# Performance work log

Measured on AMD Instinct MI355X. Metric: run time of the kernel, lower is better.

Reference implementation:

```python
import jax, jax.numpy as jnp
import numpy as np

NU, NM, FEAT, E, EL, H, ED, C = 50000, 20000, 32, 262144, 100000, 512, 7, 7


def _seg_mean(msg, dst, n):
    # scatter-mean aggregation (PyG SAGEConv default aggr='mean'; empty segments -> 0)
    s = jax.ops.segment_sum(msg, dst, num_segments=n)
    cnt = jax.ops.segment_sum(jnp.ones(dst.shape, msg.dtype), dst, num_segments=n)
    return s / jnp.maximum(cnt, 1.0)[:, None]


def _conv(x_src, x_dst, ei, ea, lw, lb, rw, ew, eb):
    # EdgeSAGEConv: message = x_j + edge_lin(edge_attr); out = lin_l(mean-aggr) + lin_r(x_dst)
    msg = x_src[ei[0]] + ea @ ew + eb            # [E, H]
    agg = _seg_mean(msg, ei[1], x_dst.shape[0])  # [N_dst, H]
    return agg @ lw + lb + x_dst @ rw


def setup_inputs() -> dict:
    key = jax.random.key(0)
    ks = iter(jax.random.split(key, 40))

    def rn(shape, scale=1.0):
        return jax.random.normal(next(ks), shape, jnp.float32) * scale

    inp = {}
    inp["movie_x"] = rn((NM, FEAT))
    inp["user_emb_w"] = rn((NU, H))
    inp["movie_emb_w"] = rn((NM, H))
    inp["movie_lin_w"] = rn((FEAT, H), FEAT ** -0.5)
    inp["movie_lin_b"] = jnp.zeros((H,), jnp.float32)
    inp["edge_attr_um"] = rn((E, ED))
    inp["edge_attr_mu"] = rn((E, ED))
    for p in ("mu1", "um1", "mu2", "um2"):
        inp[p + "_lin_l_w"] = rn((H, H), H ** -0.5)
        inp[p + "_lin_l_b"] = jnp.zeros((H,), jnp.float32)
        inp[p + "_lin_r_w"] = rn((H, H), H ** -0.5)
        inp[p + "_edge_w"] = rn((ED, H), ED ** -0.5)
        inp[p + "_edge_b"] = jnp.zeros((H,), jnp.float32)
    inp["cls_w"] = rn((2 * H, C), (2 * H) ** -0.5)
    inp["cls_b"] = jnp.zeros((C,), jnp.float32)
    inp["edge_index_um"] = jnp.stack([
        jax.random.randint(next(ks), (E,), 0, NU),
        jax.random.randint(next(ks), (E,), 0, NM)])
    inp["edge_index_mu"] = jnp.stack([
        jax.random.randint(next(ks), (E,), 0, NM),
        jax.random.randint(next(ks), (E,), 0, NU)])
    inp["edge_label_index"] = jnp.stack([
        jax.random.randint(next(ks), (EL,), 0, NU),
        jax.random.randint(next(ks), (EL,), 0, NM)])
    return inp


def reference(movie_x, user_emb_w, movie_emb_w, movie_lin_w, movie_lin_b,
              edge_attr_um, edge_attr_mu,
              mu1_lin_l_w, mu1_lin_l_b, mu1_lin_r_w, mu1_edge_w, mu1_edge_b,
              um1_lin_l_w, um1_lin_l_b, um1_lin_r_w, um1_edge_w, um1_edge_b,
              mu2_lin_l_w, mu2_lin_l_b, mu2_lin_r_w, mu2_edge_w, mu2_edge_b,
              um2_lin_l_w, um2_lin_l_b, um2_lin_r_w, um2_edge_w, um2_edge_b,
              cls_w, cls_b,
              edge_index_um, edge_index_mu, edge_label_index):
    # node encoders (node_id == arange -> embedding table used directly)
    x_u = user_emb_w                                             # [NU, H]
    x_m = movie_x @ movie_lin_w + movie_lin_b + movie_emb_w      # [NM, H]
    # hetero layer 1 (one edge type per destination node type)
    u1 = jax.nn.relu(_conv(x_m, x_u, edge_index_mu, edge_attr_mu,
                           mu1_lin_l_w, mu1_lin_l_b, mu1_lin_r_w, mu1_edge_w, mu1_edge_b))
    m1 = jax.nn.relu(_conv(x_u, x_m, edge_index_um, edge_attr_um,
                           um1_lin_l_w, um1_lin_l_b, um1_lin_r_w, um1_edge_w, um1_edge_b))
    # hetero layer 2
    u2 = _conv(m1, u1, edge_index_mu, edge_attr_mu,
               mu2_lin_l_w, mu2_lin_l_b, mu2_lin_r_w, mu2_edge_w, mu2_edge_b)
    m2 = _conv(u1, m1, edge_index_um, edge_attr_um,
               um2_lin_l_w, um2_lin_l_b, um2_lin_r_w, um2_edge_w, um2_edge_b)
    # edge classifier
    feat = jnp.concatenate([u2[edge_label_index[0]], m2[edge_label_index[1]]], axis=-1)
    return feat @ cls_w + cls_b
```

## Files before the change

kernel.cpp:

```cpp
#include <hip/hip_runtime.h>
#include <hip/hip_bf16.h>

#define NUU 50000
#define NMM 20000
#define NT (NUU + NMM)
#define FEAT 32
#define NE 262144
#define NEL 100000
#define HD 512
#define EDIM 7
#define NC 7

typedef __hip_bfloat16 bf16;
typedef __attribute__((ext_vector_type(8))) short short8;
typedef __attribute__((ext_vector_type(4))) float f32x4;

__device__ __forceinline__ float b2f(unsigned short u)
{
  return __uint_as_float((unsigned)u << 16);
}
__device__ __forceinline__ unsigned short f2bbits(float x)
{
  __hip_bfloat16 h = __float2bfloat16(x);
  return *reinterpret_cast<unsigned short*>(&h);
}
__device__ __forceinline__ float2 ld2(const float* p) { return *(const float2*)p; }
__device__ __forceinline__ void st2b(bf16* p, float x, float y)
{
  ushort2 u = make_ushort2(f2bbits(x), f2bbits(y));
  *(ushort2*)p = u;
}
__device__ __forceinline__ void gload16(const void* g, void* l)
{
  __builtin_amdgcn_global_load_lds(
      (const __attribute__((address_space(1))) void*)g,
      (__attribute__((address_space(3))) void*)l, 16, 0, 0);
}

__global__ __launch_bounds__(256) void phase1_k(
    const float* __restrict__ mx, const float* __restrict__ W,
    const float* __restrict__ b, const float* __restrict__ emb,
    bf16* __restrict__ xm, const float* __restrict__ uin, bf16* __restrict__ ubf,
    const float* __restrict__ lwA, const float* __restrict__ rwA, bf16* __restrict__ WcA,
    const float* __restrict__ lwB, const float* __restrict__ rwB, bf16* __restrict__ WcB,
    const int* __restrict__ dmu, const int* __restrict__ dum, int* __restrict__ cnt)
{
  const int tid = threadIdx.x;
  const int bx = blockIdx.x;
  if (bx < 1024) {
    const int c0 = 2 * tid;
    float2 wreg[FEAT];
#pragma unroll
    for (int k = 0; k < FEAT; ++k) wreg[k] = ld2(&W[(size_t)k * HD + c0]);
    const float2 bv = ld2(&b[c0]);
    __shared__ float xr[FEAT];
    for (int m = bx; m < NMM; m += 1024) {
      if (tid < FEAT) xr[tid] = mx[(size_t)m * FEAT + tid];
      __syncthreads();
      float2 e2 = ld2(&emb[(size_t)m * HD + c0]);
      float s0 = bv.x + e2.x, s1 = bv.y + e2.y;
#pragma unroll
      for (int k = 0; k < FEAT; ++k) {
        s0 += xr[k] * wreg[k].x;
        s1 += xr[k] * wreg[k].y;
      }
      st2b(&xm[(size_t)m * HD + c0], s0, s1);
      __syncthreads();
    }
  } else if (bx < 2048) {
    const int n4 = NUU * HD / 4;
    for (int i = (bx - 1024) * 256 + tid; i < n4; i += 1024 * 256) {
      float4 v = *(const float4*)&uin[4 * (size_t)i];
      ushort4 u = make_ushort4(f2bbits(v.x), f2bbits(v.y), f2bbits(v.z), f2bbits(v.w));
      *(ushort4*)&ubf[4 * (size_t)i] = u;
    }
  } else if (bx < 3072) {
    const int b2 = bx - 2048;
    const int side = b2 >> 9;
    const int rem = b2 & 511;
    const float* lw = side ? lwB : lwA;
    const float* rw = side ? rwB : rwA;
    bf16* Wcat = side ? WcB : WcA;
    __shared__ float s[32][33];
    const int tx = tid & 31;
    const int ty = tid >> 5;
    const int nt = (rem & 15) * 32;
    const int kt = (rem >> 4) * 32;
#pragma unroll
    for (int q = 0; q < 4; ++q) {
      int k = kt + q * 8 + ty;
      int n = nt + tx;
      float v = (k < HD) ? lw[(size_t)k * HD + n] : rw[(size_t)(k - HD) * HD + n];
      s[q * 8 + ty][tx] = v;
    }
    __syncthreads();
#pragma unroll
    for (int q = 0; q < 4; ++q) {
      int n = nt + q * 8 + ty;
      int k = kt + tx;
      Wcat[(size_t)n * (2 * HD) + k] = __float2bfloat16(s[tx][q * 8 + ty]);
    }
  } else {
    for (int i = (bx - 3072) * 256 + tid; i < NE; i += 1024 * 256) {
      atomicAdd(&cnt[dmu[i]], 1);
      atomicAdd(&cnt[NUU + dum[i]], 1);
    }
  }
}

__global__ __launch_bounds__(512) void scanA_projw_k(
    const int* __restrict__ in, int* __restrict__ out, int* __restrict__ bsum, int n,
    int GN,
    const float* __restrict__ lwA, const float* __restrict__ rwA,
    const float* __restrict__ lbA,
    const float* __restrict__ lwB, const float* __restrict__ rwB,
    const float* __restrict__ lbB, const float* __restrict__ clsW,
    float* __restrict__ WlA, float* __restrict__ WrA, float* __restrict__ ccA,
    float* __restrict__ WlB, float* __restrict__ WrB, float* __restrict__ ccB)
{
  const int tid = threadIdx.x;
  if ((int)blockIdx.x < GN) {
    __shared__ int s[512];
    const int i = blockIdx.x * 512 + tid;
    int v = (i < n) ? in[i] : 0;
    s[tid] = v;
    __syncthreads();
    for (int d = 1; d < 512; d <<= 1) {
      int t = (tid >= d) ? s[tid - d] : 0;
      __syncthreads();
      s[tid] += t;
      __syncthreads();
    }
    if (i < n) out[i] = s[tid] - v;
    if (tid == 511) bsum[blockIdx.x] = s[511];
    return;
  }
  const int unit = (blockIdx.x - GN) * 8 + (tid >> 6);
  if (unit >= 2 * (HD + 1)) return;
  const int side = unit / (HD + 1);
  const int k = unit % (HD + 1);
  const int l = tid & 63;
  const float* lw = side ? lwB : lwA;
  const float* rw = side ? rwB : rwA;
  const float* lb = side ? lbB : lbA;
  const float* cw = clsW + (side ? (size_t)HD * NC : 0);
  float* Wl = side ? WlB : WlA;
  float* Wr = side ? WrB : WrA;
  float* cc = side ? ccB : ccA;
  if (k < HD) {
    float aL[NC] = {0, 0, 0, 0, 0, 0, 0};
    float aR[NC] = {0, 0, 0, 0, 0, 0, 0};
    for (int j = l; j < HD; j += 64) {
      float a = lw[(size_t)k * HD + j];
      float b = rw[(size_t)k * HD + j];
#pragma unroll
      for (int c = 0; c < NC; ++c) {
        float w = cw[(size_t)j * NC + c];
        aL[c] += a * w;
        aR[c] += b * w;
      }
    }
#pragma unroll
    for (int c = 0; c < NC; ++c)
      for (int s2 = 32; s2; s2 >>= 1) {
        aL[c] += __shfl_xor(aL[c], s2);
        aR[c] += __shfl_xor(aR[c], s2);
      }
    if (l == 0) {
#pragma unroll
      for (int c = 0; c < NC; ++c) {
        Wl[k * NC + c] = aL[c];
        Wr[k * NC + c] = aR[c];
      }
    }
  } else {
    float a0[NC] = {0, 0, 0, 0, 0, 0, 0};
    for (int j = l; j < HD; j += 64) {
      float a = lb[j];
#pragma unroll
      for (int c = 0; c < NC; ++c) a0[c] += a * cw[(size_t)j * NC + c];
    }
#pragma unroll
    for (int c = 0; c < NC; ++c)
      for (int s2 = 32; s2; s2 >>= 1) a0[c] += __shfl_xor(a0[c], s2);
    if (l == 0) {
#pragma unroll
      for (int c = 0; c < NC; ++c) cc[c] = a0[c];
    }
  }
}

__global__ __launch_bounds__(256) void scanB_p2w2t_k(
    int* __restrict__ bsum, int nb,
    const float* __restrict__ ewA, const float* __restrict__ ebA,
    const float* __restrict__ WlA, float* __restrict__ ewPA, float* __restrict__ ebPA,
    const float* __restrict__ ewB, const float* __restrict__ ebB,
    const float* __restrict__ WlB, float* __restrict__ ewPB, float* __restrict__ ebPB,
    const float* __restrict__ WAu, const float* __restrict__ WBu, bf16* __restrict__ W2u,
    const float* __restrict__ WAm, const float* __restrict__ WBm, bf16* __restrict__ W2m)
{
  const int tid = threadIdx.x;
  if (blockIdx.x == 0) {
    __shared__ int s[256];
    int v = (tid < nb) ? bsum[tid] : 0;
    s[tid] = v;
    __syncthreads();
    for (int d = 1; d < 256; d <<= 1) {
      int t = (tid >= d) ? s[tid - d] : 0;
      __syncthreads();
      s[tid] += t;
      __syncthreads();
    }
    if (tid < nb) bsum[tid] = s[tid] - v;
    return;
  }
  const int b = blockIdx.x - 1;
  if (b < 4) {
    const int side = b >> 1;
    const float* ew = side ? ewB : ewA;
    const float* ebv = side ? ebB : ebA;
    const float* Wl = side ? WlB : WlA;
    float* ewP = side ? ewPB : ewPA;
    float* ebP = side ? ebPB : ebPA;
    const int j = (b & 1) * 4 + (tid >> 6);
    const int l = tid & 63;
    const float* __restrict__ src = (j < 7) ? &ew[(size_t)j * HD] : ebv;
    float acc[NC] = {0, 0, 0, 0, 0, 0, 0};
    for (int k = l; k < HD; k += 64) {
      float v = src[k];
#pragma unroll
      for (int c = 0; c < NC; ++c) acc[c] += v * Wl[(size_t)k * NC + c];
    }
#pragma unroll
    for (int c = 0; c < NC; ++c)
      for (int s2 = 32; s2; s2 >>= 1) acc[c] += __shfl_xor(acc[c], s2);
    if (l == 0) {
      if (j < 7) {
#pragma unroll
        for (int c = 0; c < NC; ++c) ewP[j * 8 + c] = acc[c];
        ewP[j * 8 + 7] = 0.f;
      } else {
#pragma unroll
        for (int c = 0; c < NC; ++c) ebP[c] = acc[c];
        ebP[7] = 0.f;
      }
    }
  } else {
    int idx = (b - 4) * 256 + tid;
    const int side = idx >= 16 * HD;
    if (side) idx -= 16 * HD;
    const float* WA = side ? WAm : WAu;
    const float* WB = side ? WBm : WBu;
    bf16* W2t = side ? W2m : W2u;
    int n = idx >> 9;
    int k = idx & (HD - 1);
    float v = 0.f;
    if (n < 7) v = WA[k * NC + n];
    else if (n >= 8 && n < 15) v = WB[k * NC + (n - 8)];
    W2t[(size_t)n * HD + k] = __float2bfloat16(v);
  }
}

__global__ __launch_bounds__(512) void scan_c512(int* __restrict__ out,
                                                 const int* __restrict__ bsum, int n)
{
  const int i = blockIdx.x * 512 + threadIdx.x;
  if (i < n) out[i] += bsum[blockIdx.x];
}

__global__ void fill2_k(const int* __restrict__ smu, const int* __restrict__ dmu,
                        const int* __restrict__ sum_, const int* __restrict__ dum,
                        const int* __restrict__ off, int* __restrict__ fill,
                        int2* __restrict__ csr2)
{
  for (int i = blockIdx.x * blockDim.x + threadIdx.x; i < NE; i += gridDim.x * blockDim.x) {
    int d0 = dmu[i];
    int p0 = off[d0] + atomicAdd(&fill[d0], 1);
    csr2[p0] = make_int2(smu[i], i);
    int d1 = NUU + dum[i];
    int p1 = off[d1] + atomicAdd(&fill[d1], 1);
    csr2[p1] = make_int2(sum_[i], i);
  }
}

__global__ __launch_bounds__(256) void spmm_all_k(
    const bf16* __restrict__ x_m, const bf16* __restrict__ ue_bf,
    const int2* __restrict__ csr2, const int* __restrict__ off,
    const int* __restrict__ cnt,
    const float* __restrict__ eaMU, const float* __restrict__ eaUM,
    const float* __restrict__ ew_u, const float* __restrict__ eb_u,
    const float* __restrict__ ew_m, const float* __restrict__ eb_m,
    float* __restrict__ eaSum, bf16* __restrict__ t)
{
  const int lane = threadIdx.x & 63;
  const int d = blockIdx.x * 4 + (threadIdx.x >> 6);
  if (d >= NT) return;
  const int user = (d < NUU);
  const bf16* __restrict__ xsrc = user ? x_m : ue_bf;
  const float* __restrict__ eaG = user ? eaMU : eaUM;
  const float* __restrict__ ew = user ? ew_u : ew_m;
  const float* __restrict__ eb = user ? eb_u : eb_m;
  const int deg = cnt[d];
  const int start = off[d];
  const int c0 = lane * 8;
  float acc[8] = {0.f, 0.f, 0.f, 0.f, 0.f, 0.f, 0.f, 0.f};
  float eacc = 0.f;
  int i = 0;
  for (; i + 3 < deg; i += 4) {
    int2 e0 = csr2[start + i], e1 = csr2[start + i + 1];
    int2 e2 = csr2[start + i + 2], e3 = csr2[start + i + 3];
    short8 v0 = *(const short8*)&xsrc[(size_t)e0.x * HD + c0];
    short8 v1 = *(const short8*)&xsrc[(size_t)e1.x * HD + c0];
    short8 v2 = *(const short8*)&xsrc[(size_t)e2.x * HD + c0];
    short8 v3 = *(const short8*)&xsrc[(size_t)e3.x * HD + c0];
    if (lane < 7)
      eacc += (eaG[(size_t)e0.y * EDIM + lane] + eaG[(size_t)e1.y * EDIM + lane]) +
              (eaG[(size_t)e2.y * EDIM + lane] + eaG[(size_t)e3.y * EDIM + lane]);
#pragma unroll
    for (int j = 0; j < 8; ++j)
      acc[j] += (b2f((unsigned short)v0[j]) + b2f((unsigned short)v1[j])) +
                (b2f((unsigned short)v2[j]) + b2f((unsigned short)v3[j]));
  }
  for (; i < deg; ++i) {
    int2 e = csr2[start + i];
    short8 v = *(const short8*)&xsrc[(size_t)e.x * HD + c0];
    if (lane < 7) eacc += eaG[(size_t)e.y * EDIM + lane];
#pragma unroll
    for (int j = 0; j < 8; ++j) acc[j] += b2f((unsigned short)v[j]);
  }
  if (lane < 8) eaSum[(size_t)d * 8 + lane] = (lane < 7) ? eacc : 0.f;
  short8 sv;
  if (deg > 0) {
    const float inv = 1.f / (float)deg;
    float es[8] = {0.f, 0.f, 0.f, 0.f, 0.f, 0.f, 0.f, 0.f};
#pragma unroll
    for (int j = 0; j < NC; ++j) {
      const float av = __shfl(eacc, j);
      const float* __restrict__ wr = &ew[(size_t)j * HD + c0];
#pragma unroll
      for (int jj = 0; jj < 8; ++jj) es[jj] += av * wr[jj];
    }
#pragma unroll
    for (int jj = 0; jj < 8; ++jj)
      sv[jj] = (short)f2bbits((acc[jj] + es[jj]) * inv + eb[c0 + jj]);
  } else {
#pragma unroll
    for (int jj = 0; jj < 8; ++jj) sv[jj] = (short)f2bbits(0.f);
  }
  *(short8*)&t[(size_t)d * HD + c0] = sv;
}

__global__ __launch_bounds__(256) void agg_all_k(
    const float* __restrict__ Pab, const int2* __restrict__ csr2,
    const int* __restrict__ off, const int* __restrict__ cnt,
    const float* __restrict__ eaSum,
    const float* __restrict__ ewP_u, const float* __restrict__ ebP_u,
    const float* __restrict__ cc_u, const float* __restrict__ ewP_m,
    const float* __restrict__ ebP_m, const float* __restrict__ cc_m,
    float* __restrict__ Pu, float* __restrict__ Pm)
{
  const int g = threadIdx.x >> 3;
  const int cl = threadIdx.x & 7;
  const int d = blockIdx.x * 32 + g;
  if (d >= NT) return;
  const int user = (d < NUU);
  const size_t srcbase = user ? (size_t)NUU : 0;
  const float* ewP = user ? ewP_u : ewP_m;
  const float* ebP = user ? ebP_u : ebP_m;
  const float* cc = user ? cc_u : cc_m;
  float* P = user ? Pu : Pm;
  const int dl = user ? d : d - NUU;
  const int deg = cnt[d];
  const int start = off[d];
  float a = 0.f;
  int i = 0;
  for (; i + 1 < deg; i += 2) {
    int s0 = csr2[start + i].x, s1 = csr2[start + i + 1].x;
    a += Pab[(srcbase + s0) * 16 + cl] + Pab[(srcbase + s1) * 16 + cl];
  }
  if (i < deg) a += Pab[(srcbase + csr2[start + i].x) * 16 + cl];
  float r = Pab[(size_t)d * 16 + 8 + cl] + ((cl < 7) ? cc[cl] : 0.f);
  if (deg > 0) {
    float inv = 1.f / (float)deg;
    float es = 0.f;
#pragma unroll
    for (int j = 0; j < NC; ++j) es += eaSum[(size_t)d * 8 + j] * ewP[j * 8 + cl];
    r += (a + es) * inv + ebP[cl];
  }
  if (cl < 7) P[(size_t)dl * NC + cl] = r;
}

__global__ __launch_bounds__(256) void gemm_all_k(
    const bf16* __restrict__ tbuf, const bf16* __restrict__ ue_bf,
    const bf16* __restrict__ x_m, const bf16* __restrict__ Wcat_u,
    const bf16* __restrict__ Wcat_m, const float* __restrict__ bias_u,
    const float* __restrict__ bias_m, const bf16* __restrict__ W2t_u,
    const bf16* __restrict__ W2t_m, float* __restrict__ Pab, int nwgU)
{
  __shared__ __align__(16) char lds[34816];
  const int tid = threadIdx.x;
  const int lane = tid & 63;
  const int wid = tid >> 6;
  const int wr = wid >> 1, wc = wid & 1;
  const int lr = lane & 15, lk = lane >> 4;

  const int nwg = gridDim.x;
  const int orig = blockIdx.x;
  const int q = nwg >> 3, r8 = nwg & 7;
  const int xcd = orig & 7, pos = orig >> 3;
  const int wg = (xcd < r8) ? xcd * (q + 1) + pos : r8 * (q + 1) + (xcd - r8) * q + pos;

  const int user = (wg < nwgU);
  const int wl = user ? wg : wg - nwgU;
  const bf16* __restrict__ A1 = user ? tbuf : tbuf + (size_t)NUU * HD;
  const bf16* __restrict__ A2 = user ? ue_bf : x_m;
  const bf16* __restrict__ Wcat = user ? Wcat_u : Wcat_m;
  const float* __restrict__ bias = user ? bias_u : bias_m;
  const bf16* __restrict__ W2t = user ? W2t_u : W2t_m;
  const int M = user ? NUU : NMM;
  const size_t rowbase = user ? 0 : (size_t)NUU;

  const int mt = wl >> 2, nt = wl & 3;
  const int m0 = mt * 128;
  const int n0 = nt * 128;

  const int srow = tid >> 2;
  const int sslot = tid & 3;

  f32x4 acc[4][4];
#pragma unroll
  for (int i = 0; i < 4; ++i)
#pragma unroll
    for (int j = 0; j < 4; ++j) acc[i][j] = (f32x4){0.f, 0.f, 0.f, 0.f};

  int gr0 = m0 + srow;       if (gr0 >= M) gr0 = M - 1;
  int gr1 = m0 + srow + 64;  if (gr1 >= M) gr1 = M - 1;
  const size_t aoff0 = (size_t)gr0 * HD + 8 * sslot;
  const size_t aoff1 = (size_t)gr1 * HD + 8 * sslot;
  const size_t boff0 = (size_t)(n0 + srow) * (2 * HD) + 8 * sslot;
  const size_t boff1 = (size_t)(n0 + srow + 64) * (2 * HD) + 8 * sslot;

  for (int ks = 0; ks < 32; ++ks) {
    const int k0 = ks * 32;
    const bf16* __restrict__ Ap = (k0 < HD) ? A1 : A2;
    const int ac = k0 & (HD - 1);
    gload16(Ap + aoff0 + ac, &lds[tid * 16]);
    gload16(Ap + aoff1 + ac, &lds[4096 + tid * 16]);
    gload16(Wcat + boff0 + k0, &lds[8192 + tid * 16]);
    gload16(Wcat + boff1 + k0, &lds[12288 + tid * 16]);
    __syncthreads();

    short8 af[4], bfr[4];
#pragma unroll
    for (int mf = 0; mf < 4; ++mf)
      af[mf] = *(const short8*)&lds[(wr * 64 + mf * 16 + lr) * 64 + lk * 16];
#pragma unroll
    for (int nf = 0; nf < 4; ++nf)
      bfr[nf] = *(const short8*)&lds[8192 + (wc * 64 + nf * 16 + lr) * 64 + lk * 16];
#pragma unroll
    for (int mf = 0; mf < 4; ++mf)
#pragma unroll
      for (int nf = 0; nf < 4; ++nf)
        acc[mf][nf] = __builtin_amdgcn_mfma_f32_16x16x32_bf16(
            af[mf], bfr[nf], acc[mf][nf], 0, 0, 0);
    __syncthreads();
  }

  bf16* zs = (bf16*)lds;
  const int ZLD = 136;
#pragma unroll
  for (int nf = 0; nf < 4; ++nf) {
    const int col_l = wc * 64 + nf * 16 + lr;
    const float bv = bias[n0 + col_l];
#pragma unroll
    for (int mf = 0; mf < 4; ++mf) {
      const int row_l = wr * 64 + mf * 16 + lk * 4;
#pragma unroll
      for (int r = 0; r < 4; ++r) {
        float v = fmaxf(acc[mf][nf][r] + bv, 0.f);
        zs[(size_t)(row_l + r) * ZLD + col_l] = __float2bfloat16(v);
      }
    }
  }
  __syncthreads();

  const int strip = wid * 32;
  f32x4 p0 = {0.f, 0.f, 0.f, 0.f}, p1 = {0.f, 0.f, 0.f, 0.f};
#pragma unroll
  for (int kk = 0; kk < 4; ++kk) {
    short8 bfg = *(const short8*)&W2t[(size_t)lr * HD + n0 + kk * 32 + 8 * lk];
    short8 a0 = *(const short8*)&zs[(size_t)(strip + lr) * ZLD + kk * 32 + 8 * lk];
    short8 a1 = *(const short8*)&zs[(size_t)(strip + 16 + lr) * ZLD + kk * 32 + 8 * lk];
    p0 = __builtin_amdgcn_mfma_f32_16x16x32_bf16(a0, bfg, p0, 0, 0, 0);
    p1 = __builtin_amdgcn_mfma_f32_16x16x32_bf16(a1, bfg, p1, 0, 0, 0);
  }
#pragma unroll
  for (int r = 0; r < 4; ++r) {
    int row0 = m0 + strip + lk * 4 + r;
    if (row0 < M) atomicAdd(&Pab[(rowbase + row0) * 16 + lr], p0[r]);
    int row1 = m0 + strip + 16 + lk * 4 + r;
    if (row1 < M) atomicAdd(&Pab[(rowbase + row1) * 16 + lr], p1[r]);
  }
}

__global__ void gather_out_k(const float* __restrict__ Pu, const float* __restrict__ Pm,
                             const int* __restrict__ eli, const float* __restrict__ cb,
                             float* __restrict__ out)
{
  const int i = blockIdx.x * 256 + threadIdx.x;
  if (i >= NEL * NC) return;
  int e = i / NC;
  int c = i - e * NC;
  out[i] = Pu[(size_t)eli[e] * NC + c] + Pm[(size_t)eli[NEL + e] * NC + c] + cb[c];
}

static inline char* bump(char*& p, size_t bytes)
{
  char* r = p;
  p += (bytes + 255) & ~(size_t)255;
  return r;
}

extern "C" void kernel_launch(void* const* d_in, const int* in_sizes, int n_in,
                              void* d_out, int out_size, void* d_ws, size_t ws_size,
                              hipStream_t stream)
{
  const float* movie_x   = (const float*)d_in[0];
  const float* user_emb  = (const float*)d_in[1];
  const float* movie_emb = (const float*)d_in[2];
  const float* mlw       = (const float*)d_in[3];
  const float* mlb       = (const float*)d_in[4];
  const float* ea_um     = (const float*)d_in[5];
  const float* ea_mu     = (const float*)d_in[6];
  const float* mu1_lw = (const float*)d_in[7];
  const float* mu1_lb = (const float*)d_in[8];
  const float* mu1_rw = (const float*)d_in[9];
  const float* mu1_ew = (const float*)d_in[10];
  const float* mu1_eb = (const float*)d_in[11];
  const float* um1_lw = (const float*)d_in[12];
  const float* um1_lb = (const float*)d_in[13];
  const float* um1_rw = (const float*)d_in[14];
  const float* um1_ew = (const float*)d_in[15];
  const float* um1_eb = (const float*)d_in[16];
  const float* mu2_lw = (const float*)d_in[17];
  const float* mu2_lb = (const float*)d_in[18];
  const float* mu2_rw = (const float*)d_in[19];
  const float* mu2_ew = (const float*)d_in[20];
  const float* mu2_eb = (const float*)d_in[21];
  const float* um2_lw = (const float*)d_in[22];
  const float* um2_lb = (const float*)d_in[23];
  const float* um2_rw = (const float*)d_in[24];
  const float* um2_ew = (const float*)d_in[25];
  const float* um2_eb = (const float*)d_in[26];
  const float* cls_w  = (const float*)d_in[27];
  const float* cls_b  = (const float*)d_in[28];
  const int*   ei_um  = (const int*)d_in[29];
  const int*   ei_mu  = (const int*)d_in[30];
  const int*   eli    = (const int*)d_in[31];
  float* out = (float*)d_out;

  char* w = (char*)d_ws;
  char* zbase = w;
  int* cf     = (int*)bump(w, (size_t)2 * NT * 4);
  int* cnt    = cf;
  int* fill   = cf + NT;
  float* Pab  = (float*)bump(w, (size_t)NT * 16 * 4);
  size_t zbytes = (size_t)(w - zbase);
  float* eaSum = (float*)bump(w, (size_t)NT * 8 * 4);
  bf16* x_m   = (bf16*)bump(w, (size_t)NMM * HD * 2);
  bf16* tbuf  = (bf16*)bump(w, (size_t)NT * HD * 2);
  bf16* ue_bf = (bf16*)bump(w, (size_t)NUU * HD * 2);
  bf16* Wcat_u1 = (bf16*)bump(w, (size_t)HD * 2 * HD * 2);
  bf16* Wcat_m1 = (bf16*)bump(w, (size_t)HD * 2 * HD * 2);
  float* Pu   = (float*)bump(w, (size_t)NUU * NC * 4);
  float* Pm   = (float*)bump(w, (size_t)NMM * NC * 4);
  float* Wl_u = (float*)bump(w, (size_t)HD * NC * 4);
  float* Wr_u = (float*)bump(w, (size_t)HD * NC * 4);
  float* cc_u = (float*)bump(w, 64 * 4);
  float* Wl_m = (float*)bump(w, (size_t)HD * NC * 4);
  float* Wr_m = (float*)bump(w, (size_t)HD * NC * 4);
  float* cc_m = (float*)bump(w, 64 * 4);
  bf16* W2t_u = (bf16*)bump(w, (size_t)16 * HD * 2);
  bf16* W2t_m = (bf16*)bump(w, (size_t)16 * HD * 2);
  float* ewP_u = (float*)bump(w, 64 * 4);
  float* ebP_u = (float*)bump(w, 64 * 4);
  float* ewP_m = (float*)bump(w, 64 * 4);
  float* ebP_m = (float*)bump(w, 64 * 4);
  int* off    = (int*)bump(w, (size_t)NT * 4);
  int* bsum   = (int*)bump(w, 256 * 4);
  int2* csr2  = (int2*)bump(w, (size_t)2 * NE * 8);

  const int GN = (NT + 511) / 512;
  const int PJB = (2 * (HD + 1) + 7) / 8;

  hipMemsetAsync(zbase, 0, zbytes, stream);

  phase1_k<<<4096, 256, 0, stream>>>(movie_x, mlw, mlb, movie_emb, x_m,
                                     user_emb, ue_bf,
                                     mu1_lw, mu1_rw, Wcat_u1,
                                     um1_lw, um1_rw, Wcat_m1,
                                     ei_mu + NE, ei_um + NE, cnt);

  scanA_projw_k<<<GN + PJB, 512, 0, stream>>>(cnt, off, bsum, NT, GN,
                                              mu2_lw, mu2_rw, mu2_lb,
                                              um2_lw, um2_rw, um2_lb, cls_w,
                                              Wl_u, Wr_u, cc_u, Wl_m, Wr_m, cc_m);

  scanB_p2w2t_k<<<69, 256, 0, stream>>>(bsum, GN,
                                        mu2_ew, mu2_eb, Wl_u, ewP_u, ebP_u,
                                        um2_ew, um2_eb, Wl_m, ewP_m, ebP_m,
                                        Wl_m, Wr_u, W2t_u, Wl_u, Wr_m, W2t_m);

  scan_c512<<<GN, 512, 0, stream>>>(off, bsum, NT);
  fill2_k<<<1024, 256, 0, stream>>>(ei_mu, ei_mu + NE, ei_um, ei_um + NE,
                                    off, fill, csr2);

  spmm_all_k<<<(NT + 3) / 4, 256, 0, stream>>>(x_m, ue_bf, csr2, off, cnt,
                                               ea_mu, ea_um,
                                               mu1_ew, mu1_eb, um1_ew, um1_eb,
                                               eaSum, tbuf);

  const int nwgU = ((NUU + 127) / 128) * 4;
  const int nwgM = ((NMM + 127) / 128) * 4;
  gemm_all_k<<<nwgU + nwgM, 256, 0, stream>>>(tbuf, ue_bf, x_m, Wcat_u1, Wcat_m1,
                                              mu1_lb, um1_lb, W2t_u, W2t_m,
                                              Pab, nwgU);

  agg_all_k<<<(NT + 31) / 32, 256, 0, stream>>>(Pab, csr2, off, cnt, eaSum,
                                                ewP_u, ebP_u, cc_u,
                                                ewP_m, ebP_m, cc_m, Pu, Pm);

  gather_out_k<<<(NEL * NC + 255) / 256, 256, 0, stream>>>(Pu, Pm, eli, cls_b, out);
}
```

Baseline: 330.6 us.

## Overlap CSR fill, SpMM and GEMM across user/movie halves via fused kernels

Splits the CSR fill, the SpMM and the GEMM into user and movie halves. Independent work from different stages now runs in the same launch: the movie-side CSR fill runs alongside the user SpMM, and the movie SpMM runs alongside the user GEMM. The GEMM epilogue is also reworked to stage the ReLU output in LDS in two passes, which halves LDS usage (17 KB instead of 34 KB) and should allow higher occupancy. The cost is an extra launch, more branch-divergent heterogeneous blocks, and a serial final GEMM over only the movie rows.

```diff
diff --git a/kernel.cpp b/kernel.cpp
--- a/kernel.cpp
+++ b/kernel.cpp
@@ -268,33 +268,36 @@
   if (i < n) out[i] += bsum[blockIdx.x];
 }
 
-__global__ void fill2_k(const int* __restrict__ smu, const int* __restrict__ dmu,
-                        const int* __restrict__ sum_, const int* __restrict__ dum,
+__device__ __forceinline__ void fill_half(const int* __restrict__ src,
+                                          const int* __restrict__ dst, int dofs,
+                                          const int* __restrict__ off,
+                                          int* __restrict__ fill,
+                                          int2* __restrict__ csr2,
+                                          int bx, int nblocks, int tid)
+{
+  for (int i = bx * 256 + tid; i < NE; i += nblocks * 256) {
+    int d = dofs + dst[i];
+    int p = off[d] + atomicAdd(&fill[d], 1);
+    csr2[p] = make_int2(src[i], i);
+  }
+}
+
+__global__ void fillu_k(const int* __restrict__ smu, const int* __restrict__ dmu,
                         const int* __restrict__ off, int* __restrict__ fill,
                         int2* __restrict__ csr2)
 {
-  for (int i = blockIdx.x * blockDim.x + threadIdx.x; i < NE; i += gridDim.x * blockDim.x) {
-    int d0 = dmu[i];
-    int p0 = off[d0] + atomicAdd(&fill[d0], 1);
-    csr2[p0] = make_int2(smu[i], i);
-    int d1 = NUU + dum[i];
-    int p1 = off[d1] + atomicAdd(&fill[d1], 1);
-    csr2[p1] = make_int2(sum_[i], i);
-  }
-}
-
-__global__ __launch_bounds__(256) void spmm_all_k(
-    const bf16* __restrict__ x_m, const bf16* __restrict__ ue_bf,
+  fill_half(smu, dmu, 0, off, fill, csr2, blockIdx.x, gridDim.x, threadIdx.x);
+}
+
+__device__ __forceinline__ void spmm_body(
+    int d, const bf16* __restrict__ x_m, const bf16* __restrict__ ue_bf,
     const int2* __restrict__ csr2, const int* __restrict__ off,
     const int* __restrict__ cnt,
     const float* __restrict__ eaMU, const float* __restrict__ eaUM,
     const float* __restrict__ ew_u, const float* __restrict__ eb_u,
     const float* __restrict__ ew_m, const float* __restrict__ eb_m,
-    float* __restrict__ eaSum, bf16* __restrict__ t)
-{
-  const int lane = threadIdx.x & 63;
-  const int d = blockIdx.x * 4 + (threadIdx.x >> 6);
-  if (d >= NT) return;
+    float* __restrict__ eaSum, bf16* __restrict__ t, int lane)
+{
   const int user = (d < NUU);
   const bf16* __restrict__ xsrc = user ? x_m : ue_bf;
   const float* __restrict__ eaG = user ? eaMU : eaUM;
@@ -350,6 +353,152 @@
   *(short8*)&t[(size_t)d * HD + c0] = sv;
 }
 
+__global__ __launch_bounds__(256) void spmmU_fillM_k(
+    const bf16* __restrict__ x_m, const bf16* __restrict__ ue_bf,
+    const int2* __restrict__ csr2, const int* __restrict__ off,
+    const int* __restrict__ cnt,
+    const float* __restrict__ eaMU, const float* __restrict__ eaUM,
+    const float* __restrict__ ew_u, const float* __restrict__ eb_u,
+    const float* __restrict__ ew_m, const float* __restrict__ eb_m,
+    float* __restrict__ eaSum, bf16* __restrict__ t, int nspmm,
+    const int* __restrict__ sum_, const int* __restrict__ dum,
+    int* __restrict__ fill, int2* __restrict__ csr2w)
+{
+  if ((int)blockIdx.x < nspmm) {
+    const int d = blockIdx.x * 4 + (threadIdx.x >> 6);
+    if (d < NUU)
+      spmm_body(d, x_m, ue_bf, csr2, off, cnt, eaMU, eaUM,
+                ew_u, eb_u, ew_m, eb_m, eaSum, t, threadIdx.x & 63);
+  } else {
+    fill_half(sum_, dum, NUU, off, fill, csr2w,
+              blockIdx.x - nspmm, gridDim.x - nspmm, threadIdx.x);
+  }
+}
+
+__device__ __forceinline__ void gemm_body(
+    const bf16* __restrict__ A1, const bf16* __restrict__ A2,
+    const bf16* __restrict__ Wcat, const float* __restrict__ bias,
+    const bf16* __restrict__ W2t, float* __restrict__ Pab,
+    int M, size_t rowbase, int orig, int nwg, char* lds)
+{
+  const int tid = threadIdx.x;
+  const int lane = tid & 63;
+  const int wid = tid >> 6;
+  const int wr = wid >> 1, wc = wid & 1;
+  const int lr = lane & 15, lk = lane >> 4;
+
+  const int q = nwg >> 3, r8 = nwg & 7;
+  const int xcd = orig & 7, pos = orig >> 3;
+  const int wg = (xcd < r8) ? xcd * (q + 1) + pos : r8 * (q + 1) + (xcd - r8) * q + pos;
+
+  const int mt = wg >> 2, nt = wg & 3;
+  const int m0 = mt * 128;
+  const int n0 = nt * 128;
+
+  const int srow = tid >> 2;
+  const int sslot = tid & 3;
+
+  f32x4 acc[4][4];
+#pragma unroll
+  for (int i = 0; i < 4; ++i)
+#pragma unroll
+    for (int j = 0; j < 4; ++j) acc[i][j] = (f32x4){0.f, 0.f, 0.f, 0.f};
+
+  int gr0 = m0 + srow;       if (gr0 >= M) gr0 = M - 1;
+  int gr1 = m0 + srow + 64;  if (gr1 >= M) gr1 = M - 1;
+  const size_t aoff0 = (size_t)gr0 * HD + 8 * sslot;
+  const size_t aoff1 = (size_t)gr1 * HD + 8 * sslot;
+  const size_t boff0 = (size_t)(n0 + srow) * (2 * HD) + 8 * sslot;
+  const size_t boff1 = (size_t)(n0 + srow + 64) * (2 * HD) + 8 * sslot;
+
+  for (int ks = 0; ks < 32; ++ks) {
+    const int k0 = ks * 32;
+    const bf16* __restrict__ Ap = (k0 < HD) ? A1 : A2;
+    const int ac = k0 & (HD - 1);
+    gload16(Ap + aoff0 + ac, &lds[tid * 16]);
+    gload16(Ap + aoff1 + ac, &lds[4096 + tid * 16]);
+    gload16(Wcat + boff0 + k0, &lds[8192 + tid * 16]);
+    gload16(Wcat + boff1 + k0, &lds[12288 + tid * 16]);
+    __syncthreads();
+
+    short8 af[4], bfr[4];
+#pragma unroll
+    for (int mf = 0; mf < 4; ++mf)
+      af[mf] = *(const short8*)&lds[(wr * 64 + mf * 16 + lr) * 64 + lk * 16];
+#pragma unroll
+    for (int nf = 0; nf < 4; ++nf)
+      bfr[nf] = *(const short8*)&lds[8192 + (wc * 64 + nf * 16 + lr) * 64 + lk * 16];
+#pragma unroll
+    for (int mf = 0; mf < 4; ++mf)
+#pragma unroll
+      for (int nf = 0; nf < 4; ++nf)
+        acc[mf][nf] = __builtin_amdgcn_mfma_f32_16x16x32_bf16(
+            af[mf], bfr[nf], acc[mf][nf], 0, 0, 0);
+    __syncthreads();
+  }
+
+  bf16* zs = (bf16*)lds;
+  const int ZLD = 136;
+#pragma unroll
+  for (int pass = 0; pass < 2; ++pass) {
+    if (wr == pass) {
+#pragma unroll
+      for (int nf = 0; nf < 4; ++nf) {
+        const int col_l = wc * 64 + nf * 16 + lr;
+        const float bv = bias[n0 + col_l];
+#pragma unroll
+        for (int mf = 0; mf < 4; ++mf) {
+          const int row_l = mf * 16 + lk * 4;
+#pragma unroll
+          for (int r = 0; r < 4; ++r) {
+            float v = fmaxf(acc[mf][nf][r] + bv, 0.f);
+            zs[(size_t)(row_l + r) * ZLD + col_l] = __float2bfloat16(v);
+          }
+        }
+      }
+    }
+    __syncthreads();
+    f32x4 p0 = {0.f, 0.f, 0.f, 0.f};
+#pragma unroll
+    for (int kk = 0; kk < 4; ++kk) {
+      short8 bfg = *(const short8*)&W2t[(size_t)lr * HD + n0 + kk * 32 + 8 * lk];
+      short8 a0 = *(const short8*)&zs[(size_t)(wid * 16 + lr) * ZLD + kk * 32 + 8 * lk];
+      p0 = __builtin_amdgcn_mfma_f32_16x16x32_bf16(a0, bfg, p0, 0, 0, 0);
+    }
+#pragma unroll
+    for (int r = 0; r < 4; ++r) {
+      int row = m0 + pass * 64 + wid * 16 + lk * 4 + r;
+      if (row < M) atomicAdd(&Pab[(rowbase + row) * 16 + lr], p0[r]);
+    }
+    __syncthreads();
+  }
+}
+
+__global__ __launch_bounds__(256) void gemm_spmm_k(
+    const bf16* __restrict__ A1, const bf16* __restrict__ A2,
+    const bf16* __restrict__ Wcat, const float* __restrict__ bias,
+    const bf16* __restrict__ W2t, float* __restrict__ Pab, int M, int rowbase,
+    int nwgGemm,
+    const bf16* __restrict__ x_m, const bf16* __restrict__ ue_bf,
+    const int2* __restrict__ csr2, const int* __restrict__ off,
+    const int* __restrict__ cnt,
+    const float* __restrict__ eaMU, const float* __restrict__ eaUM,
+    const float* __restrict__ ew_u, const float* __restrict__ eb_u,
+    const float* __restrict__ ew_m, const float* __restrict__ eb_m,
+    float* __restrict__ eaSum, bf16* __restrict__ t, int dbase)
+{
+  __shared__ __align__(16) char lds[17408];
+  if ((int)blockIdx.x < nwgGemm) {
+    gemm_body(A1, A2, Wcat, bias, W2t, Pab, M, (size_t)rowbase,
+              blockIdx.x, nwgGemm, lds);
+  } else {
+    const int d = dbase + (blockIdx.x - nwgGemm) * 4 + (threadIdx.x >> 6);
+    if (d < NT)
+      spmm_body(d, x_m, ue_bf, csr2, off, cnt, eaMU, eaUM,
+                ew_u, eb_u, ew_m, eb_m, eaSum, t, threadIdx.x & 63);
+  }
+}
+
 __global__ __launch_bounds__(256) void agg_all_k(
     const float* __restrict__ Pab, const int2* __restrict__ csr2,
     const int* __restrict__ off, const int* __restrict__ cnt,
@@ -388,119 +537,6 @@
     r += (a + es) * inv + ebP[cl];
   }
   if (cl < 7) P[(size_t)dl * NC + cl] = r;
-}
-
-__global__ __launch_bounds__(256) void gemm_all_k(
-    const bf16* __restrict__ tbuf, const bf16* __restrict__ ue_bf,
-    const bf16* __restrict__ x_m, const bf16* __restrict__ Wcat_u,
-    const bf16* __restrict__ Wcat_m, const float* __restrict__ bias_u,
-    const float* __restrict__ bias_m, const bf16* __restrict__ W2t_u,
-    const bf16* __restrict__ W2t_m, float* __restrict__ Pab, int nwgU)
-{
-  __shared__ __align__(16) char lds[34816];
-  const int tid = threadIdx.x;
-  const int lane = tid & 63;
-  const int wid = tid >> 6;
-  const int wr = wid >> 1, wc = wid & 1;
-  const int lr = lane & 15, lk = lane >> 4;
-
-  const int nwg = gridDim.x;
-  const int orig = blockIdx.x;
-  const int q = nwg >> 3, r8 = nwg & 7;
-  const int xcd = orig & 7, pos = orig >> 3;
-  const int wg = (xcd < r8) ? xcd * (q + 1) + pos : r8 * (q + 1) + (xcd - r8) * q + pos;
-
-  const int user = (wg < nwgU);
-  const int wl = user ? wg : wg - nwgU;
-  const bf16* __restrict__ A1 = user ? tbuf : tbuf + (size_t)NUU * HD;
-  const bf16* __restrict__ A2 = user ? ue_bf : x_m;
-  const bf16* __restrict__ Wcat = user ? Wcat_u : Wcat_m;
-  const float* __restrict__ bias = user ? bias_u : bias_m;
-  const bf16* __restrict__ W2t = user ? W2t_u : W2t_m;
-  const int M = user ? NUU : NMM;
-  const size_t rowbase = user ? 0 : (size_t)NUU;
-
-  const int mt = wl >> 2, nt = wl & 3;
-  const int m0 = mt * 128;
-  const int n0 = nt * 128;
-
-  const int srow = tid >> 2;
-  const int sslot = tid & 3;
-
-  f32x4 acc[4][4];
-#pragma unroll
-  for (int i = 0; i < 4; ++i)
-#pragma unroll
-    for (int j = 0; j < 4; ++j) acc[i][j] = (f32x4){0.f, 0.f, 0.f, 0.f};
-
-  int gr0 = m0 + srow;       if (gr0 >= M) gr0 = M - 1;
-  int gr1 = m0 + srow + 64;  if (gr1 >= M) gr1 = M - 1;
-  const size_t aoff0 = (size_t)gr0 * HD + 8 * sslot;
-  const size_t aoff1 = (size_t)gr1 * HD + 8 * sslot;
-  const size_t boff0 = (size_t)(n0 + srow) * (2 * HD) + 8 * sslot;
-  const size_t boff1 = (size_t)(n0 + srow + 64) * (2 * HD) + 8 * sslot;
-
-  for (int ks = 0; ks < 32; ++ks) {
-    const int k0 = ks * 32;
-    const bf16* __restrict__ Ap = (k0 < HD) ? A1 : A2;
-    const int ac = k0 & (HD - 1);
-    gload16(Ap + aoff0 + ac, &lds[tid * 16]);
-    gload16(Ap + aoff1 + ac, &lds[4096 + tid * 16]);
-    gload16(Wcat + boff0 + k0, &lds[8192 + tid * 16]);
-    gload16(Wcat + boff1 + k0, &lds[12288 + tid * 16]);
-    __syncthreads();
-
-    short8 af[4], bfr[4];
-#pragma unroll
-    for (int mf = 0; mf < 4; ++mf)
-      af[mf] = *(const short8*)&lds[(wr * 64 + mf * 16 + lr) * 64 + lk * 16];
-#pragma unroll
-    for (int nf = 0; nf < 4; ++nf)
-      bfr[nf] = *(const short8*)&lds[8192 + (wc * 64 + nf * 16 + lr) * 64 + lk * 16];
-#pragma unroll
-    for (int mf = 0; mf < 4; ++mf)
-#pragma unroll
-      for (int nf = 0; nf < 4; ++nf)
-        acc[mf][nf] = __builtin_amdgcn_mfma_f32_16x16x32_bf16(
-            af[mf], bfr[nf], acc[mf][nf], 0, 0, 0);
-    __syncthreads();
-  }
-
-  bf16* zs = (bf16*)lds;
-  const int ZLD = 136;
-#pragma unroll
-  for (int nf = 0; nf < 4; ++nf) {
-    const int col_l = wc * 64 + nf * 16 + lr;
-    const float bv = bias[n0 + col_l];
-#pragma unroll
-    for (int mf = 0; mf < 4; ++mf) {
-      const int row_l = wr * 64 + mf * 16 + lk * 4;
-#pragma unroll
-      for (int r = 0; r < 4; ++r) {
-        float v = fmaxf(acc[mf][nf][r] + bv, 0.f);
-        zs[(size_t)(row_l + r) * ZLD + col_l] = __float2bfloat16(v);
-      }
-    }
-  }
-  __syncthreads();
-
-  const int strip = wid * 32;
-  f32x4 p0 = {0.f, 0.f, 0.f, 0.f}, p1 = {0.f, 0.f, 0.f, 0.f};
-#pragma unroll
-  for (int kk = 0; kk < 4; ++kk) {
-    short8 bfg = *(const short8*)&W2t[(size_t)lr * HD + n0 + kk * 32 + 8 * lk];
-    short8 a0 = *(const short8*)&zs[(size_t)(strip + lr) * ZLD + kk * 32 + 8 * lk];
-    short8 a1 = *(const short8*)&zs[(size_t)(strip + 16 + lr) * ZLD + kk * 32 + 8 * lk];
-    p0 = __builtin_amdgcn_mfma_f32_16x16x32_bf16(a0, bfg, p0, 0, 0, 0);
-    p1 = __builtin_amdgcn_mfma_f32_16x16x32_bf16(a1, bfg, p1, 0, 0, 0);
-  }
-#pragma unroll
-  for (int r = 0; r < 4; ++r) {
-    int row0 = m0 + strip + lk * 4 + r;
-    if (row0 < M) atomicAdd(&Pab[(rowbase + row0) * 16 + lr], p0[r]);
-    int row1 = m0 + strip + 16 + lk * 4 + r;
-    if (row1 < M) atomicAdd(&Pab[(rowbase + row1) * 16 + lr], p1[r]);
-  }
 }
 
 __global__ void gather_out_k(const float* __restrict__ Pu, const float* __restrict__ Pm,
@@ -612,19 +648,27 @@
                                         Wl_m, Wr_u, W2t_u, Wl_u, Wr_m, W2t_m);
 
   scan_c512<<<GN, 512, 0, stream>>>(off, bsum, NT);
-  fill2_k<<<1024, 256, 0, stream>>>(ei_mu, ei_mu + NE, ei_um, ei_um + NE,
-                                    off, fill, csr2);
-
-  spmm_all_k<<<(NT + 3) / 4, 256, 0, stream>>>(x_m, ue_bf, csr2, off, cnt,
-                                               ea_mu, ea_um,
-                                               mu1_ew, mu1_eb, um1_ew, um1_eb,
-                                               eaSum, tbuf);
+
+  fillu_k<<<1024, 256, 0, stream>>>(ei_mu, ei_mu + NE, off, fill, csr2);
+
+  const int nspmmU = (NUU + 3) / 4;
+  spmmU_fillM_k<<<nspmmU + 512, 256, 0, stream>>>(
+      x_m, ue_bf, csr2, off, cnt, ea_mu, ea_um,
+      mu1_ew, mu1_eb, um1_ew, um1_eb, eaSum, tbuf, nspmmU,
+      ei_um, ei_um + NE, fill, csr2);
 
   const int nwgU = ((NUU + 127) / 128) * 4;
+  const int nspmmM = (NMM + 3) / 4;
+  gemm_spmm_k<<<nwgU + nspmmM, 256, 0, stream>>>(
+      tbuf, ue_bf, Wcat_u1, mu1_lb, W2t_u, Pab, NUU, 0, nwgU,
+      x_m, ue_bf, csr2, off, cnt, ea_mu, ea_um,
+      mu1_ew, mu1_eb, um1_ew, um1_eb, eaSum, tbuf, NUU);
+
   const int nwgM = ((NMM + 127) / 128) * 4;
-  gemm_all_k<<<nwgU + nwgM, 256, 0, stream>>>(tbuf, ue_bf, x_m, Wcat_u1, Wcat_m1,
-                                              mu1_lb, um1_lb, W2t_u, W2t_m,
-                                              Pab, nwgU);
+  gemm_spmm_k<<<nwgM, 256, 0, stream>>>(
+      tbuf + (size_t)NUU * HD, x_m, Wcat_m1, um1_lb, W2t_m, Pab, NMM, NUU, nwgM,
+      x_m, ue_bf, csr2, off, cnt, ea_mu, ea_um,
+      mu1_ew, mu1_eb, um1_ew, um1_eb, eaSum, tbuf, NT);
 
   agg_all_k<<<(NT + 31) / 32, 256, 0, stream>>>(Pab, csr2, off, cnt, eaSum,
                                                 ewP_u, ebP_u, cc_u,
```

Result: slower. 348.0 us (+5.2%).

## Split CSR fill by edge type and overlap movie fill with user SpMM

Applied to the files above, without the earlier changes.

The combined CSR fill kernel is split into a user-destination fill and a movie-destination fill. The movie fill now runs as extra blocks inside the user-side SpMM kernel, and a separate kernel handles the movie-side SpMM afterwards. The goal is to hide the atomic scatter of the second fill behind the gather-heavy user aggregation. The cost is one more kernel launch and blocks with uneven work sharing the GPU. The gemm kernel is only moved within the file.

```diff
diff --git a/kernel.cpp b/kernel.cpp
--- a/kernel.cpp
+++ b/kernel.cpp
@@ -268,33 +268,36 @@
   if (i < n) out[i] += bsum[blockIdx.x];
 }
 
-__global__ void fill2_k(const int* __restrict__ smu, const int* __restrict__ dmu,
-                        const int* __restrict__ sum_, const int* __restrict__ dum,
+__device__ __forceinline__ void fill_half(const int* __restrict__ src,
+                                          const int* __restrict__ dst, int dofs,
+                                          const int* __restrict__ off,
+                                          int* __restrict__ fill,
+                                          int2* __restrict__ csr2,
+                                          int bx, int nblocks, int tid)
+{
+  for (int i = bx * 256 + tid; i < NE; i += nblocks * 256) {
+    int d = dofs + dst[i];
+    int p = off[d] + atomicAdd(&fill[d], 1);
+    csr2[p] = make_int2(src[i], i);
+  }
+}
+
+__global__ void fillu_k(const int* __restrict__ smu, const int* __restrict__ dmu,
                         const int* __restrict__ off, int* __restrict__ fill,
                         int2* __restrict__ csr2)
 {
-  for (int i = blockIdx.x * blockDim.x + threadIdx.x; i < NE; i += gridDim.x * blockDim.x) {
-    int d0 = dmu[i];
-    int p0 = off[d0] + atomicAdd(&fill[d0], 1);
-    csr2[p0] = make_int2(smu[i], i);
-    int d1 = NUU + dum[i];
-    int p1 = off[d1] + atomicAdd(&fill[d1], 1);
-    csr2[p1] = make_int2(sum_[i], i);
-  }
-}
-
-__global__ __launch_bounds__(256) void spmm_all_k(
-    const bf16* __restrict__ x_m, const bf16* __restrict__ ue_bf,
+  fill_half(smu, dmu, 0, off, fill, csr2, blockIdx.x, gridDim.x, threadIdx.x);
+}
+
+__device__ __forceinline__ void spmm_body(
+    int d, const bf16* __restrict__ x_m, const bf16* __restrict__ ue_bf,
     const int2* __restrict__ csr2, const int* __restrict__ off,
     const int* __restrict__ cnt,
     const float* __restrict__ eaMU, const float* __restrict__ eaUM,
     const float* __restrict__ ew_u, const float* __restrict__ eb_u,
     const float* __restrict__ ew_m, const float* __restrict__ eb_m,
-    float* __restrict__ eaSum, bf16* __restrict__ t)
-{
-  const int lane = threadIdx.x & 63;
-  const int d = blockIdx.x * 4 + (threadIdx.x >> 6);
-  if (d >= NT) return;
+    float* __restrict__ eaSum, bf16* __restrict__ t, int lane)
+{
   const int user = (d < NUU);
   const bf16* __restrict__ xsrc = user ? x_m : ue_bf;
   const float* __restrict__ eaG = user ? eaMU : eaUM;
@@ -350,6 +353,156 @@
   *(short8*)&t[(size_t)d * HD + c0] = sv;
 }
 
+__global__ __launch_bounds__(256) void spmmU_fillM_k(
+    const bf16* __restrict__ x_m, const bf16* __restrict__ ue_bf,
+    const int2* __restrict__ csr2, const int* __restrict__ off,
+    const int* __restrict__ cnt,
+    const float* __restrict__ eaMU, const float* __restrict__ eaUM,
+    const float* __restrict__ ew_u, const float* __restrict__ eb_u,
+    const float* __restrict__ ew_m, const float* __restrict__ eb_m,
+    float* __restrict__ eaSum, bf16* __restrict__ t, int nspmm,
+    const int* __restrict__ sum_, const int* __restrict__ dum,
+    int* __restrict__ fill, int2* __restrict__ csr2w)
+{
+  if ((int)blockIdx.x < nspmm) {
+    const int d = blockIdx.x * 4 + (threadIdx.x >> 6);
+    if (d < NUU)
+      spmm_body(d, x_m, ue_bf, csr2, off, cnt, eaMU, eaUM,
+                ew_u, eb_u, ew_m, eb_m, eaSum, t, threadIdx.x & 63);
+  } else {
+    fill_half(sum_, dum, NUU, off, fill, csr2w,
+              blockIdx.x - nspmm, gridDim.x - nspmm, threadIdx.x);
+  }
+}
+
+__global__ __launch_bounds__(256) void spmmM_k(
+    const bf16* __restrict__ x_m, const bf16* __restrict__ ue_bf,
+    const int2* __restrict__ csr2, const int* __restrict__ off,
+    const int* __restrict__ cnt,
+    const float* __restrict__ eaMU, const float* __restrict__ eaUM,
+    const float* __restrict__ ew_u, const float* __restrict__ eb_u,
+    const float* __restrict__ ew_m, const float* __restrict__ eb_m,
+    float* __restrict__ eaSum, bf16* __restrict__ t)
+{
+  const int d = NUU + blockIdx.x * 4 + (threadIdx.x >> 6);
+  if (d < NT)
+    spmm_body(d, x_m, ue_bf, csr2, off, cnt, eaMU, eaUM,
+              ew_u, eb_u, ew_m, eb_m, eaSum, t, threadIdx.x & 63);
+}
+
+__global__ __launch_bounds__(256) void gemm_all_k(
+    const bf16* __restrict__ tbuf, const bf16* __restrict__ ue_bf,
+    const bf16* __restrict__ x_m, const bf16* __restrict__ Wcat_u,
+    const bf16* __restrict__ Wcat_m, const float* __restrict__ bias_u,
+    const float* __restrict__ bias_m, const bf16* __restrict__ W2t_u,
+    const bf16* __restrict__ W2t_m, float* __restrict__ Pab, int nwgU)
+{
+  __shared__ __align__(16) char lds[34816];
+  const int tid = threadIdx.x;
+  const int lane = tid & 63;
+  const int wid = tid >> 6;
+  const int wr = wid >> 1, wc = wid & 1;
+  const int lr = lane & 15, lk = lane >> 4;
+
+  const int nwg = gridDim.x;
+  const int orig = blockIdx.x;
+  const int q = nwg >> 3, r8 = nwg & 7;
+  const int xcd = orig & 7, pos = orig >> 3;
+  const int wg = (xcd < r8) ? xcd * (q + 1) + pos : r8 * (q + 1) + (xcd - r8) * q + pos;
+
+  const int user = (wg < nwgU);
+  const int wl = user ? wg : wg - nwgU;
+  const bf16* __restrict__ A1 = user ? tbuf : tbuf + (size_t)NUU * HD;
+  const bf16* __restrict__ A2 = user ? ue_bf : x_m;
+  const bf16* __restrict__ Wcat = user ? Wcat_u : Wcat_m;
+  const float* __restrict__ bias = user ? bias_u : bias_m;
+  const bf16* __restrict__ W2t = user ? W2t_u : W2t_m;
+  const int M = user ? NUU : NMM;
+  const size_t rowbase = user ? 0 : (size_t)NUU;
+
+  const int mt = wl >> 2, nt = wl & 3;
+  const int m0 = mt * 128;
+  const int n0 = nt * 128;
+
+  const int srow = tid >> 2;
+  const int sslot = tid & 3;
+
+  f32x4 acc[4][4];
+#pragma unroll
+  for (int i = 0; i < 4; ++i)
+#pragma unroll
+    for (int j = 0; j < 4; ++j) acc[i][j] = (f32x4){0.f, 0.f, 0.f, 0.f};
+
+  int gr0 = m0 + srow;       if (gr0 >= M) gr0 = M - 1;
+  int gr1 = m0 + srow + 64;  if (gr1 >= M) gr1 = M - 1;
+  const size_t aoff0 = (size_t)gr0 * HD + 8 * sslot;
+  const size_t aoff1 = (size_t)gr1 * HD + 8 * sslot;
+  const size_t boff0 = (size_t)(n0 + srow) * (2 * HD) + 8 * sslot;
+  const size_t boff1 = (size_t)(n0 + srow + 64) * (2 * HD) + 8 * sslot;
+
+  for (int ks = 0; ks < 32; ++ks) {
+    const int k0 = ks * 32;
+    const bf16* __restrict__ Ap = (k0 < HD) ? A1 : A2;
+    const int ac = k0 & (HD - 1);
+    gload16(Ap + aoff0 + ac, &lds[tid * 16]);
+    gload16(Ap + aoff1 + ac, &lds[4096 + tid * 16]);
+    gload16(Wcat + boff0 + k0, &lds[8192 + tid * 16]);
+    gload16(Wcat + boff1 + k0, &lds[12288 + tid * 16]);
+    __syncthreads();
+
+    short8 af[4], bfr[4];
+#pragma unroll
+    for (int mf = 0; mf < 4; ++mf)
+      af[mf] = *(const short8*)&lds[(wr * 64 + mf * 16 + lr) * 64 + lk * 16];
+#pragma unroll
+    for (int nf = 0; nf < 4; ++nf)
+      bfr[nf] = *(const short8*)&lds[8192 + (wc * 64 + nf * 16 + lr) * 64 + lk * 16];
+#pragma unroll
+    for (int mf = 0; mf < 4; ++mf)
+#pragma unroll
+      for (int nf = 0; nf < 4; ++nf)
+        acc[mf][nf] = __builtin_amdgcn_mfma_f32_16x16x32_bf16(
+            af[mf], bfr[nf], acc[mf][nf], 0, 0, 0);
+    __syncthreads();
+  }
+
+  bf16* zs = (bf16*)lds;
+  const int ZLD = 136;
+#pragma unroll
+  for (int nf = 0; nf < 4; ++nf) {
+    const int col_l = wc * 64 + nf * 16 + lr;
+    const float bv = bias[n0 + col_l];
+#pragma unroll
+    for (int mf = 0; mf < 4; ++mf) {
+      const int row_l = wr * 64 + mf * 16 + lk * 4;
+#pragma unroll
+      for (int r = 0; r < 4; ++r) {
+        float v = fmaxf(acc[mf][nf][r] + bv, 0.f);
+        zs[(size_t)(row_l + r) * ZLD + col_l] = __float2bfloat16(v);
+      }
+    }
+  }
+  __syncthreads();
+
+  const int strip = wid * 32;
+  f32x4 p0 = {0.f, 0.f, 0.f, 0.f}, p1 = {0.f, 0.f, 0.f, 0.f};
+#pragma unroll
+  for (int kk = 0; kk < 4; ++kk) {
+    short8 bfg = *(const short8*)&W2t[(size_t)lr * HD + n0 + kk * 32 + 8 * lk];
+    short8 a0 = *(const short8*)&zs[(size_t)(strip + lr) * ZLD + kk * 32 + 8 * lk];
+    short8 a1 = *(const short8*)&zs[(size_t)(strip + 16 + lr) * ZLD + kk * 32 + 8 * lk];
+    p0 = __builtin_amdgcn_mfma_f32_16x16x32_bf16(a0, bfg, p0, 0, 0, 0);
+    p1 = __builtin_amdgcn_mfma_f32_16x16x32_bf16(a1, bfg, p1, 0, 0, 0);
+  }
+#pragma unroll
+  for (int r = 0; r < 4; ++r) {
+    int row0 = m0 + strip + lk * 4 + r;
+    if (row0 < M) atomicAdd(&Pab[(rowbase + row0) * 16 + lr], p0[r]);
+    int row1 = m0 + strip + 16 + lk * 4 + r;
+    if (row1 < M) atomicAdd(&Pab[(rowbase + row1) * 16 + lr], p1[r]);
+  }
+}
+
 __global__ __launch_bounds__(256) void agg_all_k(
     const float* __restrict__ Pab, const int2* __restrict__ csr2,
     const int* __restrict__ off, const int* __restrict__ cnt,
@@ -388,119 +541,6 @@
     r += (a + es) * inv + ebP[cl];
   }
   if (cl < 7) P[(size_t)dl * NC + cl] = r;
-}
-
-__global__ __launch_bounds__(256) void gemm_all_k(
-    const bf16* __restrict__ tbuf, const bf16* __restrict__ ue_bf,
-    const bf16* __restrict__ x_m, const bf16* __restrict__ Wcat_u,
-    const bf16* __restrict__ Wcat_m, const float* __restrict__ bias_u,
-    const float* __restrict__ bias_m, const bf16* __restrict__ W2t_u,
-    const bf16* __restrict__ W2t_m, float* __restrict__ Pab, int nwgU)
-{
-  __shared__ __align__(16) char lds[34816];
-  const int tid = threadIdx.x;
-  const int lane = tid & 63;
-  const int wid = tid >> 6;
-  const int wr = wid >> 1, wc = wid & 1;
-  const int lr = lane & 15, lk = lane >> 4;
-
-  const int nwg = gridDim.x;
-  const int orig = blockIdx.x;
-  const int q = nwg >> 3, r8 = nwg & 7;
-  const int xcd = orig & 7, pos = orig >> 3;
-  const int wg = (xcd < r8) ? xcd * (q + 1) + pos : r8 * (q + 1) + (xcd - r8) * q + pos;
-
-  const int user = (wg < nwgU);
-  const int wl = user ? wg : wg - nwgU;
-  const bf16* __restrict__ A1 = user ? tbuf : tbuf + (size_t)NUU * HD;
-  const bf16* __restrict__ A2 = user ? ue_bf : x_m;
-  const bf16* __restrict__ Wcat = user ? Wcat_u : Wcat_m;
-  const float* __restrict__ bias = user ? bias_u : bias_m;
-  const bf16* __restrict__ W2t = user ? W2t_u : W2t_m;
-  const int M = user ? NUU : NMM;
-  const size_t rowbase = user ? 0 : (size_t)NUU;
-
-  const int mt = wl >> 2, nt = wl & 3;
-  const int m0 = mt * 128;
-  const int n0 = nt * 128;
-
-  const int srow = tid >> 2;
-  const int sslot = tid & 3;
-
-  f32x4 acc[4][4];
-#pragma unroll
-  for (int i = 0; i < 4; ++i)
-#pragma unroll
-    for (int j = 0; j < 4; ++j) acc[i][j] = (f32x4){0.f, 0.f, 0.f, 0.f};
-
-  int gr0 = m0 + srow;       if (gr0 >= M) gr0 = M - 1;
-  int gr1 = m0 + srow + 64;  if (gr1 >= M) gr1 = M - 1;
-  const size_t aoff0 = (size_t)gr0 * HD + 8 * sslot;
-  const size_t aoff1 = (size_t)gr1 * HD + 8 * sslot;
-  const size_t boff0 = (size_t)(n0 + srow) * (2 * HD) + 8 * sslot;
-  const size_t boff1 = (size_t)(n0 + srow + 64) * (2 * HD) + 8 * sslot;
-
-  for (int ks = 0; ks < 32; ++ks) {
-    const int k0 = ks * 32;
-    const bf16* __restrict__ Ap = (k0 < HD) ? A1 : A2;
-    const int ac = k0 & (HD - 1);
-    gload16(Ap + aoff0 + ac, &lds[tid * 16]);
-    gload16(Ap + aoff1 + ac, &lds[4096 + tid * 16]);
-    gload16(Wcat + boff0 + k0, &lds[8192 + tid * 16]);
-    gload16(Wcat + boff1 + k0, &lds[12288 + tid * 16]);
-    __syncthreads();
-
-    short8 af[4], bfr[4];
-#pragma unroll
-    for (int mf = 0; mf < 4; ++mf)
-      af[mf] = *(const short8*)&lds[(wr * 64 + mf * 16 + lr) * 64 + lk * 16];
-#pragma unroll
-    for (int nf = 0; nf < 4; ++nf)
-      bfr[nf] = *(const short8*)&lds[8192 + (wc * 64 + nf * 16 + lr) * 64 + lk * 16];
-#pragma unroll
-    for (int mf = 0; mf < 4; ++mf)
-#pragma unroll
-      for (int nf = 0; nf < 4; ++nf)
-        acc[mf][nf] = __builtin_amdgcn_mfma_f32_16x16x32_bf16(
-            af[mf], bfr[nf], acc[mf][nf], 0, 0, 0);
-    __syncthreads();
-  }
-
-  bf16* zs = (bf16*)lds;
-  const int ZLD = 136;
-#pragma unroll
-  for (int nf = 0; nf < 4; ++nf) {
-    const int col_l = wc * 64 + nf * 16 + lr;
-    const float bv = bias[n0 + col_l];
-#pragma unroll
-    for (int mf = 0; mf < 4; ++mf) {
-      const int row_l = wr * 64 + mf * 16 + lk * 4;
-#pragma unroll
-      for (int r = 0; r < 4; ++r) {
-        float v = fmaxf(acc[mf][nf][r] + bv, 0.f);
-        zs[(size_t)(row_l + r) * ZLD + col_l] = __float2bfloat16(v);
-      }
-    }
-  }
-  __syncthreads();
-
-  const int strip = wid * 32;
-  f32x4 p0 = {0.f, 0.f, 0.f, 0.f}, p1 = {0.f, 0.f, 0.f, 0.f};
-#pragma unroll
-  for (int kk = 0; kk < 4; ++kk) {
-    short8 bfg = *(const short8*)&W2t[(size_t)lr * HD + n0 + kk * 32 + 8 * lk];
-    short8 a0 = *(const short8*)&zs[(size_t)(strip + lr) * ZLD + kk * 32 + 8 * lk];
-    short8 a1 = *(const short8*)&zs[(size_t)(strip + 16 + lr) * ZLD + kk * 32 + 8 * lk];
-    p0 = __builtin_amdgcn_mfma_f32_16x16x32_bf16(a0, bfg, p0, 0, 0, 0);
-    p1 = __builtin_amdgcn_mfma_f32_16x16x32_bf16(a1, bfg, p1, 0, 0, 0);
-  }
-#pragma unroll
-  for (int r = 0; r < 4; ++r) {
-    int row0 = m0 + strip + lk * 4 + r;
-    if (row0 < M) atomicAdd(&Pab[(rowbase + row0) * 16 + lr], p0[r]);
-    int row1 = m0 + strip + 16 + lk * 4 + r;
-    if (row1 < M) atomicAdd(&Pab[(rowbase + row1) * 16 + lr], p1[r]);
-  }
 }
 
 __global__ void gather_out_k(const float* __restrict__ Pu, const float* __restrict__ Pm,
@@ -612,13 +652,18 @@
                                         Wl_m, Wr_u, W2t_u, Wl_u, Wr_m, W2t_m);
 
   scan_c512<<<GN, 512, 0, stream>>>(off, bsum, NT);
-  fill2_k<<<1024, 256, 0, stream>>>(ei_mu, ei_mu + NE, ei_um, ei_um + NE,
-                                    off, fill, csr2);
-
-  spmm_all_k<<<(NT + 3) / 4, 256, 0, stream>>>(x_m, ue_bf, csr2, off, cnt,
-                                               ea_mu, ea_um,
-                                               mu1_ew, mu1_eb, um1_ew, um1_eb,
-                                               eaSum, tbuf);
+
+  fillu_k<<<1024, 256, 0, stream>>>(ei_mu, ei_mu + NE, off, fill, csr2);
+
+  const int nspmmU = (NUU + 3) / 4;
+  spmmU_fillM_k<<<nspmmU + 512, 256, 0, stream>>>(
+      x_m, ue_bf, csr2, off, cnt, ea_mu, ea_um,
+      mu1_ew, mu1_eb, um1_ew, um1_eb, eaSum, tbuf, nspmmU,
+      ei_um, ei_um + NE, fill, csr2);
+
+  spmmM_k<<<(NMM + 3) / 4, 256, 0, stream>>>(
+      x_m, ue_bf, csr2, off, cnt, ea_mu, ea_um,
+      mu1_ew, mu1_eb, um1_ew, um1_eb, eaSum, tbuf);
 
   const int nwgU = ((NUU + 127) / 128) * 4;
   const int nwgM = ((NMM + 127) / 128) * 4;
```

Result: no change. 332.5 us (+0.5%).
